# Kernel tuning notes

Hardware: AMD Instinct MI355X
Metric: run time of the kernel (lower is better)

Reference implementation:

```python
import jax, jax.numpy as jnp
import numpy as np

N_NODES = 35
N_EDGES = 1190
N_VIEWS = 6
C1_IN, C1_OUT = 1, 256
C2_IN, C2_OUT = 256, 256
C3_IN, C3_OUT = 256, 64


def _nnconv(x, edge_attr, src, dst, nn_w, nn_b, lin_w, bias, c_in, c_out):
    """PyG NNConv with aggr='mean': per-edge MLP weight, gather-matvec-scatter."""
    # per-edge weight matrices: [E, c_in, c_out]
    W = jax.nn.relu(edge_attr @ nn_w.T + nn_b).reshape(-1, c_in, c_out)
    # gather source features and apply per-edge weight: [E, c_out]
    msg = jnp.einsum('ei,eio->eo', x[src], W)
    # scatter-mean into target nodes
    agg = jax.ops.segment_sum(msg, dst, num_segments=N_NODES)
    cnt = jax.ops.segment_sum(jnp.ones((msg.shape[0],), msg.dtype), dst,
                              num_segments=N_NODES)
    agg = agg / jnp.maximum(cnt, 1.0)[:, None]
    # root transform (lin has no bias in PyG) + conv bias
    return agg + x @ lin_w.T + bias


def setup_inputs() -> dict:
    key = jax.random.key(0)
    ks = jax.random.split(key, 16)
    s = 0.05
    x = jnp.ones((N_NODES, C1_IN), jnp.float32)
    edge_attr = jax.random.uniform(ks[0], (N_EDGES, N_VIEWS), jnp.float32)
    edge_index = jax.random.randint(ks[1], (2, N_EDGES), 0, N_NODES, jnp.int32)
    inp = {
        'x': x, 'edge_attr': edge_attr, 'edge_index': edge_index,
        'nn1_w': jax.random.normal(ks[2], (C1_IN * C1_OUT, N_VIEWS), jnp.float32) * s,
        'nn1_b': jax.random.normal(ks[3], (C1_IN * C1_OUT,), jnp.float32) * s,
        'lin1_w': jax.random.normal(ks[4], (C1_OUT, C1_IN), jnp.float32) * s,
        'b1': jax.random.normal(ks[5], (C1_OUT,), jnp.float32) * s,
        'nn2_w': jax.random.normal(ks[6], (C2_IN * C2_OUT, N_VIEWS), jnp.float32) * s,
        'nn2_b': jax.random.normal(ks[7], (C2_IN * C2_OUT,), jnp.float32) * s,
        'lin2_w': jax.random.normal(ks[8], (C2_OUT, C2_IN), jnp.float32) * s,
        'b2': jax.random.normal(ks[9], (C2_OUT,), jnp.float32) * s,
        'nn3_w': jax.random.normal(ks[10], (C3_IN * C3_OUT, N_VIEWS), jnp.float32) * s,
        'nn3_b': jax.random.normal(ks[11], (C3_IN * C3_OUT,), jnp.float32) * s,
        'lin3_w': jax.random.normal(ks[12], (C3_OUT, C3_IN), jnp.float32) * s,
        'b3': jax.random.normal(ks[13], (C3_OUT,), jnp.float32) * s,
    }
    return inp


def reference(x, edge_attr, edge_index, nn1_w, nn1_b, lin1_w, b1,
              nn2_w, nn2_b, lin2_w, b2, nn3_w, nn3_b, lin3_w, b3):
    src, dst = edge_index[0], edge_index[1]
    x = jax.nn.relu(_nnconv(x, edge_attr, src, dst, nn1_w, nn1_b, lin1_w, b1, C1_IN, C1_OUT))
    x = jax.nn.relu(_nnconv(x, edge_attr, src, dst, nn2_w, nn2_b, lin2_w, b2, C2_IN, C2_OUT))
    x = jax.nn.relu(_nnconv(x, edge_attr, src, dst, nn3_w, nn3_b, lin3_w, b3, C3_IN, C3_OUT))
    # CBT: pairwise L1 distances over feature dim -> [N, N]
    # (equivalent to repeat(35,1,1) / transpose / abs / sum since N == 35)
    cbt = jnp.abs(x[None, :, :] - x[:, None, :]).sum(-1)
    return cbt
```

## Files before the change

### kernel.cpp

```cpp
#include <hip/hip_runtime.h>


#define NN 35
#define NE 1190
#define TE 10
#define NG 119

#define OFF_AGG1 0
#define OFF_AGG2 8960
#define OFF_AGG3 17920
#define OFF_CNT  20160
#define ZERO_N   20195
#define OFF_L2T  20224
#define OFF_X2M  85760
#define OFF_X3   94720

__global__ __launch_bounds__(256) void prep_k(float* __restrict__ ws,
                                              const float* __restrict__ lin2) {
    int b = blockIdx.x, t = threadIdx.x;
    if (b < 80) {
        int idx = b * 256 + t;
        if (idx < ZERO_N) ws[idx] = 0.f;
    } else {
        int i = b - 80;
        ws[OFF_L2T + i * 256 + t] = lin2[t * 256 + i];
    }
}

__global__ __launch_bounds__(512) void msg1_k(
    const float* __restrict__ x, const float* __restrict__ ea,
    const int* __restrict__ ei, const float* __restrict__ w1,
    const float* __restrict__ b1w, float* __restrict__ agg1,
    float* __restrict__ cnt) {
    int tid = threadIdx.x;
    int e = blockIdx.x * 2 + (tid >> 8);
    int o = tid & 255;
    int src = ei[e];
    int dst = ei[NE + e];
    float xs = x[src];
    const float* eap = ea + e * 6;
    const float* w = w1 + o * 6;
    float d = b1w[o];
#pragma unroll
    for (int v = 0; v < 6; v++) d = fmaf(eap[v], w[v], d);
    atomicAdd(agg1 + dst * 256 + o, xs * fmaxf(d, 0.f));
    if (o == 0) atomicAdd(cnt + dst, 1.0f);
}

__global__ __launch_bounds__(512, 4) void msg2x1_k(
    const float* __restrict__ x, const float* __restrict__ ea,
    const int* __restrict__ ei, const float* __restrict__ lin1,
    const float* __restrict__ b1, const float* __restrict__ agg1,
    const float* __restrict__ cnt, const float* __restrict__ w2,
    const float* __restrict__ b2w, float* __restrict__ agg2) {
    __shared__ float xs[TE][256];
    __shared__ float eas[TE][6];
    __shared__ int srcs[TE], dsts[TE];
    __shared__ float part[7][TE][64];
    int tid = threadIdx.x;
    int eg = blockIdx.x >> 2, og = blockIdx.x & 3;
    int e0 = eg * TE;
    if (tid < TE) { srcs[tid] = ei[e0 + tid]; dsts[tid] = ei[NE + e0 + tid]; }
    if (tid >= 64 && tid < 64 + TE * 6) {
        int t = tid - 64;
        eas[t / 6][t % 6] = ea[e0 * 6 + t];
    }
    __syncthreads();
    for (int idx = tid; idx < TE * 256; idx += 512) {
        int te = idx >> 8, i = idx & 255;
        int s = srcs[te];
        float c = fmaxf(cnt[s], 1.f);
        float v = agg1[s * 256 + i] / c + x[s] * lin1[i] + b1[i];
        xs[te][i] = fmaxf(v, 0.f);
    }
    __syncthreads();
    int ol = tid & 63;
    int o = og * 64 + ol;
    int ic = tid >> 6;
    float eareg[TE][6];
#pragma unroll
    for (int te = 0; te < TE; te++)
#pragma unroll
        for (int v = 0; v < 6; v++) eareg[te][v] = eas[te][v];
    float acc[TE] = {};
    for (int ii = 0; ii < 32; ii++) {
        int i = ic * 32 + ii;
        const float* w = w2 + (size_t)(i * 256 + o) * 6;
        float2 wa = *(const float2*)w;
        float2 wb = *(const float2*)(w + 2);
        float2 wc = *(const float2*)(w + 4);
        float b = b2w[i * 256 + o];
#pragma unroll
        for (int te = 0; te < TE; te += 2) {
            float dx = b, dy = b;
            dx = fmaf(eareg[te][0], wa.x, dx); dy = fmaf(eareg[te + 1][0], wa.x, dy);
            dx = fmaf(eareg[te][1], wa.y, dx); dy = fmaf(eareg[te + 1][1], wa.y, dy);
            dx = fmaf(eareg[te][2], wb.x, dx); dy = fmaf(eareg[te + 1][2], wb.x, dy);
            dx = fmaf(eareg[te][3], wb.y, dx); dy = fmaf(eareg[te + 1][3], wb.y, dy);
            dx = fmaf(eareg[te][4], wc.x, dx); dy = fmaf(eareg[te + 1][4], wc.x, dy);
            dx = fmaf(eareg[te][5], wc.y, dx); dy = fmaf(eareg[te + 1][5], wc.y, dy);
            dx = fmaxf(dx, 0.f);               dy = fmaxf(dy, 0.f);
            acc[te] = fmaf(xs[te][i], dx, acc[te]);
            acc[te + 1] = fmaf(xs[te + 1][i], dy, acc[te + 1]);
        }
    }
    if (ic > 0) {
#pragma unroll
        for (int te = 0; te < TE; te++) part[ic - 1][te][ol] = acc[te];
    }
    __syncthreads();
    if (ic == 0) {
#pragma unroll
        for (int te = 0; te < TE; te++) {
            float s = acc[te];
#pragma unroll
            for (int p = 0; p < 7; p++) s += part[p][te][ol];
            atomicAdd(agg2 + dsts[te] * 256 + o, s);
        }
    }
}

__global__ __launch_bounds__(512, 4) void msg3x2_k(
    const float* __restrict__ x, const float* __restrict__ ea,
    const int* __restrict__ ei, const float* __restrict__ lin1,
    const float* __restrict__ b1, const float* __restrict__ agg1,
    const float* __restrict__ cnt, const float* __restrict__ lin2T,
    const float* __restrict__ b2, const float* __restrict__ agg2,
    const float* __restrict__ w3, const float* __restrict__ b3w,
    float* __restrict__ agg3, float* __restrict__ x2m) {
    __shared__ float x1r[TE][256];
    __shared__ float xs[TE][64];
    __shared__ float eas[TE][6];
    __shared__ int srcs[TE], dsts[TE];
    __shared__ float part[7][TE][64];
    int tid = threadIdx.x;

    if (blockIdx.x >= 476) {
        int n = blockIdx.x - 476;
        float c = fmaxf(cnt[n], 1.f);
        if (tid < 256) {
            float v = agg1[n * 256 + tid] / c + x[n] * lin1[tid] + b1[tid];
            x1r[0][tid] = fmaxf(v, 0.f);
        }
        __syncthreads();
        int o = tid & 255, ic = tid >> 8;
        float s = 0.f;
        for (int ii = 0; ii < 128; ii++) {
            int i = ic * 128 + ii;
            s = fmaf(lin2T[i * 256 + o], x1r[0][i], s);
        }
        float* p2 = &part[0][0][0];
        if (ic == 1) p2[o] = s;
        __syncthreads();
        if (ic == 0) {
            float v = agg2[n * 256 + o] / c + s + p2[o] + b2[o];
            x2m[n * 256 + o] = fmaxf(v, 0.f);
        }
        return;
    }

    int eg = blockIdx.x >> 2, ig = blockIdx.x & 3;
    int e0 = eg * TE;
    if (tid < TE) { srcs[tid] = ei[e0 + tid]; dsts[tid] = ei[NE + e0 + tid]; }
    if (tid >= 64 && tid < 64 + TE * 6) {
        int t = tid - 64;
        eas[t / 6][t % 6] = ea[e0 * 6 + t];
    }
    __syncthreads();
    for (int idx = tid; idx < TE * 256; idx += 512) {
        int te = idx >> 8, i = idx & 255;
        int s = srcs[te];
        float c = fmaxf(cnt[s], 1.f);
        float v = agg1[s * 256 + i] / c + x[s] * lin1[i] + b1[i];
        x1r[te][i] = fmaxf(v, 0.f);
    }
    __syncthreads();
    int ol = tid & 63;
    int ic = tid >> 6;
    int o2 = ig * 64 + ol;
    {
        float acc2[TE] = {};
        for (int ii = 0; ii < 32; ii++) {
            int i = ic * 32 + ii;
            float w = lin2T[i * 256 + o2];
#pragma unroll
            for (int te = 0; te < TE; te++)
                acc2[te] = fmaf(w, x1r[te][i], acc2[te]);
        }
        if (ic > 0) {
#pragma unroll
            for (int te = 0; te < TE; te++) part[ic - 1][te][ol] = acc2[te];
        }
        __syncthreads();
        if (ic == 0) {
#pragma unroll
            for (int te = 0; te < TE; te++) {
                float ssum = acc2[te];
#pragma unroll
                for (int p = 0; p < 7; p++) ssum += part[p][te][ol];
                int s = srcs[te];
                float c = fmaxf(cnt[s], 1.f);
                float v = agg2[s * 256 + o2] / c + ssum + b2[o2];
                xs[te][ol] = fmaxf(v, 0.f);
            }
        }
        __syncthreads();
    }
    float eareg[TE][6];
#pragma unroll
    for (int te = 0; te < TE; te++)
#pragma unroll
        for (int v = 0; v < 6; v++) eareg[te][v] = eas[te][v];
    float acc[TE] = {};
    for (int jj = 0; jj < 8; jj++) {
        int ii = ic * 8 + jj;
        int i = ig * 64 + ii;
        const float* w = w3 + (size_t)(i * 64 + ol) * 6;
        float2 wa = *(const float2*)w;
        float2 wb = *(const float2*)(w + 2);
        float2 wc = *(const float2*)(w + 4);
        float b = b3w[i * 64 + ol];
#pragma unroll
        for (int te = 0; te < TE; te += 2) {
            float dx = b, dy = b;
            dx = fmaf(eareg[te][0], wa.x, dx); dy = fmaf(eareg[te + 1][0], wa.x, dy);
            dx = fmaf(eareg[te][1], wa.y, dx); dy = fmaf(eareg[te + 1][1], wa.y, dy);
            dx = fmaf(eareg[te][2], wb.x, dx); dy = fmaf(eareg[te + 1][2], wb.x, dy);
            dx = fmaf(eareg[te][3], wb.y, dx); dy = fmaf(eareg[te + 1][3], wb.y, dy);
            dx = fmaf(eareg[te][4], wc.x, dx); dy = fmaf(eareg[te + 1][4], wc.x, dy);
            dx = fmaf(eareg[te][5], wc.y, dx); dy = fmaf(eareg[te + 1][5], wc.y, dy);
            dx = fmaxf(dx, 0.f);               dy = fmaxf(dy, 0.f);
            acc[te] = fmaf(xs[te][ii], dx, acc[te]);
            acc[te + 1] = fmaf(xs[te + 1][ii], dy, acc[te + 1]);
        }
    }
    if (ic > 0) {
#pragma unroll
        for (int te = 0; te < TE; te++) part[ic - 1][te][ol] = acc[te];
    }
    __syncthreads();
    if (ic == 0) {
#pragma unroll
        for (int te = 0; te < TE; te++) {
            float s = acc[te];
#pragma unroll
            for (int p = 0; p < 7; p++) s += part[p][te][ol];
            atomicAdd(agg3 + dsts[te] * 64 + ol, s);
        }
    }
}

__global__ __launch_bounds__(256) void x3_k(
    const float* __restrict__ x2m, const float* __restrict__ lin3,
    const float* __restrict__ b3, const float* __restrict__ agg3,
    const float* __restrict__ cnt, float* __restrict__ x3) {
    __shared__ float xr[256];
    __shared__ float part[3][64];
    int n = blockIdx.x, tid = threadIdx.x;
    int o = tid & 63, ic = tid >> 6;
    xr[tid] = x2m[n * 256 + tid];
    __syncthreads();
    const float4* w = (const float4*)(lin3 + (size_t)o * 256 + ic * 64);
    float s = 0.f;
#pragma unroll
    for (int k = 0; k < 16; k++) {
        float4 wv = w[k];
        int i = ic * 64 + k * 4;
        s = fmaf(wv.x, xr[i], s);
        s = fmaf(wv.y, xr[i + 1], s);
        s = fmaf(wv.z, xr[i + 2], s);
        s = fmaf(wv.w, xr[i + 3], s);
    }
    if (ic > 0) part[ic - 1][o] = s;
    __syncthreads();
    if (ic == 0) {
        float tot = s + part[0][o] + part[1][o] + part[2][o];
        float c = fmaxf(cnt[n], 1.f);
        x3[n * 64 + o] = fmaxf(agg3[n * 64 + o] / c + tot + b3[o], 0.f);
    }
}

__global__ __launch_bounds__(256) void cbt_k(const float* __restrict__ x3,
                                             float* __restrict__ out) {
    int t = blockIdx.x * 256 + threadIdx.x;
    if (t >= NN * NN) return;
    int i = t / NN, j = t % NN;
    const float* a = x3 + i * 64;
    const float* b = x3 + j * 64;
    float s = 0.f;
#pragma unroll
    for (int f = 0; f < 64; f++) s += fabsf(a[f] - b[f]);
    out[t] = s;
}

extern "C" void kernel_launch(void* const* d_in, const int* in_sizes, int n_in,
                              void* d_out, int out_size, void* d_ws, size_t ws_size,
                              hipStream_t stream) {
    const float* x    = (const float*)d_in[0];
    const float* ea   = (const float*)d_in[1];
    const int*   ei   = (const int*)d_in[2];
    const float* nn1w = (const float*)d_in[3];
    const float* nn1b = (const float*)d_in[4];
    const float* lin1 = (const float*)d_in[5];
    const float* b1   = (const float*)d_in[6];
    const float* nn2w = (const float*)d_in[7];
    const float* nn2b = (const float*)d_in[8];
    const float* lin2 = (const float*)d_in[9];
    const float* b2   = (const float*)d_in[10];
    const float* nn3w = (const float*)d_in[11];
    const float* nn3b = (const float*)d_in[12];
    const float* lin3 = (const float*)d_in[13];
    const float* b3   = (const float*)d_in[14];

    float* ws    = (float*)d_ws;
    float* agg1  = ws + OFF_AGG1;
    float* agg2  = ws + OFF_AGG2;
    float* agg3  = ws + OFF_AGG3;
    float* cnt   = ws + OFF_CNT;
    float* lin2T = ws + OFF_L2T;
    float* x2m   = ws + OFF_X2M;
    float* x3v   = ws + OFF_X3;
    float* out   = (float*)d_out;

    prep_k<<<336, 256, 0, stream>>>(ws, lin2);
    msg1_k<<<NE / 2, 512, 0, stream>>>(x, ea, ei, nn1w, nn1b, agg1, cnt);
    msg2x1_k<<<NG * 4, 512, 0, stream>>>(x, ea, ei, lin1, b1, agg1, cnt,
                                         nn2w, nn2b, agg2);
    msg3x2_k<<<NG * 4 + NN, 512, 0, stream>>>(x, ea, ei, lin1, b1, agg1, cnt,
                                              lin2T, b2, agg2, nn3w, nn3b,
                                              agg3, x2m);
    x3_k<<<NN, 256, 0, stream>>>(x2m, lin3, b3, agg3, cnt, x3v);
    cbt_k<<<(NN * NN + 255) / 256, 256, 0, stream>>>(x3v, out);
}
```

Before: 140.9 us.

## Fuse all NNConv stages into one persistent kernel with grid barriers

Replaces the six-kernel pipeline with a single persistent kernel of 238 blocks that passes through the stages using software grid barriers on an atomic counter, plus a tiny init kernel to reset the counter. Float atomics for scatter-mean are replaced by per-destination edge lists built with ballot, with per-edge messages written to workspace and gathered deterministically by destination. The layer-2 root transform no longer needs a transposed copy of lin2. This targets launch overhead and atomic contention, at the cost of spin-wait barriers that rely on all blocks being co-resident, plus extra workspace traffic for the message buffers.

```diff
diff --git a/kernel.cpp b/kernel.cpp
--- a/kernel.cpp
+++ b/kernel.cpp
@@ -3,299 +3,307 @@
 
 #define NN 35
 #define NE 1190
-#define TE 10
-#define NG 119
-
-#define OFF_AGG1 0
-#define OFF_AGG2 8960
-#define OFF_AGG3 17920
-#define OFF_CNT  20160
-#define ZERO_N   20195
-#define OFF_L2T  20224
-#define OFF_X2M  85760
-#define OFF_X3   94720
-
-__global__ __launch_bounds__(256) void prep_k(float* __restrict__ ws,
-                                              const float* __restrict__ lin2) {
-    int b = blockIdx.x, t = threadIdx.x;
-    if (b < 80) {
-        int idx = b * 256 + t;
-        if (idx < ZERO_N) ws[idx] = 0.f;
-    } else {
-        int i = b - 80;
-        ws[OFF_L2T + i * 256 + t] = lin2[t * 256 + i];
-    }
+#define NBLK 238
+#define TE2 10
+#define TE3 5
+
+#define OFF_X1    64
+#define OFF_CNT   9024
+#define OFF_ELIST 9088
+#define OFF_MP    51200
+#define OFF_MP3   660480
+#define OFF_X2    736640
+#define OFF_X3    745600
+
+__global__ __launch_bounds__(64) void init_k(unsigned* bar) {
+    if (threadIdx.x < 16) bar[threadIdx.x] = 0u;
 }
 
-__global__ __launch_bounds__(512) void msg1_k(
-    const float* __restrict__ x, const float* __restrict__ ea,
-    const int* __restrict__ ei, const float* __restrict__ w1,
-    const float* __restrict__ b1w, float* __restrict__ agg1,
-    float* __restrict__ cnt) {
-    int tid = threadIdx.x;
-    int e = blockIdx.x * 2 + (tid >> 8);
-    int o = tid & 255;
-    int src = ei[e];
-    int dst = ei[NE + e];
-    float xs = x[src];
-    const float* eap = ea + e * 6;
-    const float* w = w1 + o * 6;
-    float d = b1w[o];
-#pragma unroll
-    for (int v = 0; v < 6; v++) d = fmaf(eap[v], w[v], d);
-    atomicAdd(agg1 + dst * 256 + o, xs * fmaxf(d, 0.f));
-    if (o == 0) atomicAdd(cnt + dst, 1.0f);
+__device__ __forceinline__ void gbar(unsigned* bar, unsigned target) {
+    __syncthreads();
+    if (threadIdx.x == 0) {
+        __threadfence();
+        atomicAdd(bar, 1u);
+        while (__hip_atomic_load(bar, __ATOMIC_RELAXED,
+                                 __HIP_MEMORY_SCOPE_AGENT) < target)
+            __builtin_amdgcn_s_sleep(2);
+        __threadfence();
+    }
+    __syncthreads();
 }
 
-__global__ __launch_bounds__(512, 4) void msg2x1_k(
-    const float* __restrict__ x, const float* __restrict__ ea,
-    const int* __restrict__ ei, const float* __restrict__ lin1,
-    const float* __restrict__ b1, const float* __restrict__ agg1,
-    const float* __restrict__ cnt, const float* __restrict__ w2,
-    const float* __restrict__ b2w, float* __restrict__ agg2) {
-    __shared__ float xs[TE][256];
-    __shared__ float eas[TE][6];
-    __shared__ int srcs[TE], dsts[TE];
-    __shared__ float part[7][TE][64];
-    int tid = threadIdx.x;
-    int eg = blockIdx.x >> 2, og = blockIdx.x & 3;
-    int e0 = eg * TE;
-    if (tid < TE) { srcs[tid] = ei[e0 + tid]; dsts[tid] = ei[NE + e0 + tid]; }
-    if (tid >= 64 && tid < 64 + TE * 6) {
-        int t = tid - 64;
-        eas[t / 6][t % 6] = ea[e0 * 6 + t];
-    }
-    __syncthreads();
-    for (int idx = tid; idx < TE * 256; idx += 512) {
-        int te = idx >> 8, i = idx & 255;
-        int s = srcs[te];
-        float c = fmaxf(cnt[s], 1.f);
-        float v = agg1[s * 256 + i] / c + x[s] * lin1[i] + b1[i];
-        xs[te][i] = fmaxf(v, 0.f);
-    }
-    __syncthreads();
-    int ol = tid & 63;
-    int o = og * 64 + ol;
-    int ic = tid >> 6;
-    float eareg[TE][6];
-#pragma unroll
-    for (int te = 0; te < TE; te++)
-#pragma unroll
-        for (int v = 0; v < 6; v++) eareg[te][v] = eas[te][v];
-    float acc[TE] = {};
-    for (int ii = 0; ii < 32; ii++) {
-        int i = ic * 32 + ii;
-        const float* w = w2 + (size_t)(i * 256 + o) * 6;
-        float2 wa = *(const float2*)w;
-        float2 wb = *(const float2*)(w + 2);
-        float2 wc = *(const float2*)(w + 4);
-        float b = b2w[i * 256 + o];
-#pragma unroll
-        for (int te = 0; te < TE; te += 2) {
-            float dx = b, dy = b;
-            dx = fmaf(eareg[te][0], wa.x, dx); dy = fmaf(eareg[te + 1][0], wa.x, dy);
-            dx = fmaf(eareg[te][1], wa.y, dx); dy = fmaf(eareg[te + 1][1], wa.y, dy);
-            dx = fmaf(eareg[te][2], wb.x, dx); dy = fmaf(eareg[te + 1][2], wb.x, dy);
-            dx = fmaf(eareg[te][3], wb.y, dx); dy = fmaf(eareg[te + 1][3], wb.y, dy);
-            dx = fmaf(eareg[te][4], wc.x, dx); dy = fmaf(eareg[te + 1][4], wc.x, dy);
-            dx = fmaf(eareg[te][5], wc.y, dx); dy = fmaf(eareg[te + 1][5], wc.y, dy);
-            dx = fmaxf(dx, 0.f);               dy = fmaxf(dy, 0.f);
-            acc[te] = fmaf(xs[te][i], dx, acc[te]);
-            acc[te + 1] = fmaf(xs[te + 1][i], dy, acc[te + 1]);
-        }
-    }
-    if (ic > 0) {
-#pragma unroll
-        for (int te = 0; te < TE; te++) part[ic - 1][te][ol] = acc[te];
-    }
-    __syncthreads();
-    if (ic == 0) {
-#pragma unroll
-        for (int te = 0; te < TE; te++) {
-            float s = acc[te];
-#pragma unroll
-            for (int p = 0; p < 7; p++) s += part[p][te][ol];
-            atomicAdd(agg2 + dsts[te] * 256 + o, s);
-        }
-    }
-}
-
-__global__ __launch_bounds__(512, 4) void msg3x2_k(
-    const float* __restrict__ x, const float* __restrict__ ea,
-    const int* __restrict__ ei, const float* __restrict__ lin1,
-    const float* __restrict__ b1, const float* __restrict__ agg1,
-    const float* __restrict__ cnt, const float* __restrict__ lin2T,
-    const float* __restrict__ b2, const float* __restrict__ agg2,
+__global__ __launch_bounds__(512, 2) void mega_k(
+    float* __restrict__ ws, const float* __restrict__ x,
+    const float* __restrict__ ea, const int* __restrict__ ei,
+    const float* __restrict__ w1, const float* __restrict__ b1w,
+    const float* __restrict__ lin1, const float* __restrict__ b1,
+    const float* __restrict__ w2, const float* __restrict__ b2w,
+    const float* __restrict__ lin2, const float* __restrict__ b2,
     const float* __restrict__ w3, const float* __restrict__ b3w,
-    float* __restrict__ agg3, float* __restrict__ x2m) {
-    __shared__ float x1r[TE][256];
-    __shared__ float xs[TE][64];
-    __shared__ float eas[TE][6];
-    __shared__ int srcs[TE], dsts[TE];
-    __shared__ float part[7][TE][64];
-    int tid = threadIdx.x;
-
-    if (blockIdx.x >= 476) {
-        int n = blockIdx.x - 476;
-        float c = fmaxf(cnt[n], 1.f);
-        if (tid < 256) {
-            float v = agg1[n * 256 + tid] / c + x[n] * lin1[tid] + b1[tid];
-            x1r[0][tid] = fmaxf(v, 0.f);
-        }
-        __syncthreads();
-        int o = tid & 255, ic = tid >> 8;
-        float s = 0.f;
-        for (int ii = 0; ii < 128; ii++) {
-            int i = ic * 128 + ii;
-            s = fmaf(lin2T[i * 256 + o], x1r[0][i], s);
-        }
-        float* p2 = &part[0][0][0];
-        if (ic == 1) p2[o] = s;
+    const float* __restrict__ lin3, const float* __restrict__ b3,
+    float* __restrict__ out) {
+    __shared__ float smem[4096];
+    unsigned* bar = (unsigned*)ws;
+    const int tid = threadIdx.x;
+    const int bid = blockIdx.x;
+    int* elist_all = (int*)(ws + OFF_ELIST);
+
+    if (bid < NN) {
+        const int n = bid;
+        int* elist = elist_all + n * NE;
+        int* degS = (int*)smem;
+        if (tid < 64) {
+            int deg = 0;
+            for (int base = 0; base < NE; base += 64) {
+                const int e = base + tid;
+                const bool m = (e < NE) && (ei[NE + e] == n);
+                const unsigned long long mk = __ballot(m);
+                if (m) elist[deg + __popcll(mk & ((1ull << tid) - 1ull))] = e;
+                deg += __popcll(mk);
+            }
+            if (tid == 0) { degS[0] = deg; ws[OFF_CNT + n] = (float)deg; }
+        }
+        __syncthreads();
+        const int deg = degS[0];
+        const int o = tid & 255, ech = tid >> 8;
+        const float* wr = w1 + o * 6;
+        const float wv0 = wr[0], wv1 = wr[1], wv2 = wr[2];
+        const float wv3 = wr[3], wv4 = wr[4], wv5 = wr[5];
+        const float bb = b1w[o];
+        float a = 0.f;
+        for (int k = ech; k < deg; k += 2) {
+            const int e = elist[k];
+            const float* eap = ea + e * 6;
+            float d = bb;
+            d = fmaf(eap[0], wv0, d); d = fmaf(eap[1], wv1, d);
+            d = fmaf(eap[2], wv2, d); d = fmaf(eap[3], wv3, d);
+            d = fmaf(eap[4], wv4, d); d = fmaf(eap[5], wv5, d);
+            a = fmaf(x[ei[e]], fmaxf(d, 0.f), a);
+        }
+        float* part = smem + 1024;
+        if (ech == 1) part[o] = a;
+        __syncthreads();
+        if (ech == 0) {
+            const float c = fmaxf((float)deg, 1.f);
+            const float v = (a + part[o]) / c + x[n] * lin1[o] + b1[o];
+            ws[OFF_X1 + n * 256 + o] = fmaxf(v, 0.f);
+        }
+    }
+    gbar(bar, NBLK * 1u);
+
+    {
+        const int eg = bid >> 1, ig = bid & 1;
+        const int e0 = eg * TE2;
+        int* srcsS = (int*)smem;
+        float* easS = smem + 16;
+        float* xsS = smem + 128;
+        float* partS = smem + 1536;
+        if (tid < TE2) srcsS[tid] = ei[e0 + tid];
+        if (tid >= 64 && tid < 64 + TE2 * 6) {
+            const int t = tid - 64;
+            easS[t] = ea[e0 * 6 + t];
+        }
+        __syncthreads();
+        for (int idx = tid; idx < TE2 * 128; idx += 512) {
+            const int te = idx >> 7, il = idx & 127;
+            xsS[te * 128 + il] = ws[OFF_X1 + srcsS[te] * 256 + ig * 128 + il];
+        }
+        __syncthreads();
+        const int o = tid & 255, ich = tid >> 8;
+        float ear[TE2][6];
+#pragma unroll
+        for (int te = 0; te < TE2; te++)
+#pragma unroll
+            for (int v = 0; v < 6; v++) ear[te][v] = easS[te * 6 + v];
+        float acc[TE2] = {};
+        for (int ii = 0; ii < 64; ii++) {
+            const int il = ich * 64 + ii;
+            const int i = ig * 128 + il;
+            const float* wp = w2 + (size_t)(i * 256 + o) * 6;
+            const float2 wa = *(const float2*)wp;
+            const float2 wb = *(const float2*)(wp + 2);
+            const float2 wc = *(const float2*)(wp + 4);
+            const float b = b2w[i * 256 + o];
+#pragma unroll
+            for (int te = 0; te < TE2; te += 2) {
+                float dx = b, dy = b;
+                dx = fmaf(ear[te][0], wa.x, dx); dy = fmaf(ear[te+1][0], wa.x, dy);
+                dx = fmaf(ear[te][1], wa.y, dx); dy = fmaf(ear[te+1][1], wa.y, dy);
+                dx = fmaf(ear[te][2], wb.x, dx); dy = fmaf(ear[te+1][2], wb.x, dy);
+                dx = fmaf(ear[te][3], wb.y, dx); dy = fmaf(ear[te+1][3], wb.y, dy);
+                dx = fmaf(ear[te][4], wc.x, dx); dy = fmaf(ear[te+1][4], wc.x, dy);
+                dx = fmaf(ear[te][5], wc.y, dx); dy = fmaf(ear[te+1][5], wc.y, dy);
+                dx = fmaxf(dx, 0.f);             dy = fmaxf(dy, 0.f);
+                acc[te]   = fmaf(xsS[te * 128 + il], dx, acc[te]);
+                acc[te+1] = fmaf(xsS[(te+1) * 128 + il], dy, acc[te+1]);
+            }
+        }
+        if (ich == 1) {
+#pragma unroll
+            for (int te = 0; te < TE2; te++) partS[te * 256 + o] = acc[te];
+        }
+        __syncthreads();
+        if (ich == 0) {
+#pragma unroll
+            for (int te = 0; te < TE2; te++)
+                ws[OFF_MP + (size_t)(ig * NE + e0 + te) * 256 + o] =
+                    acc[te] + partS[te * 256 + o];
+        }
+    }
+    gbar(bar, NBLK * 2u);
+
+    if (bid < NN) {
+        const int n = bid;
+        const int deg = (int)ws[OFF_CNT + n];
+        const int* el = elist_all + n * NE;
+        float* xrowS = smem;
+        float* pA = smem + 256;
+        float* pB = smem + 512;
+        if (tid < 256) xrowS[tid] = ws[OFF_X1 + n * 256 + tid];
+        __syncthreads();
+        const int o = tid & 255, ich = tid >> 8;
+        const float4* l4 = (const float4*)(lin2 + (size_t)o * 256 + ich * 128);
+        float slin = 0.f;
+#pragma unroll
+        for (int k = 0; k < 32; k++) {
+            const float4 wv = l4[k];
+            const int i = ich * 128 + k * 4;
+            slin = fmaf(wv.x, xrowS[i], slin);
+            slin = fmaf(wv.y, xrowS[i+1], slin);
+            slin = fmaf(wv.z, xrowS[i+2], slin);
+            slin = fmaf(wv.w, xrowS[i+3], slin);
+        }
+        float sagg = 0.f;
+        const float* mpb = ws + OFF_MP + (size_t)ich * NE * 256;
+        for (int k = 0; k < deg; k++)
+            sagg += mpb[(size_t)el[k] * 256 + o];
+        if (ich == 1) { pA[o] = slin; pB[o] = sagg; }
+        __syncthreads();
+        if (ich == 0) {
+            const float c = fmaxf((float)deg, 1.f);
+            const float v = (sagg + pB[o]) / c + slin + pA[o] + b2[o];
+            ws[OFF_X2 + n * 256 + o] = fmaxf(v, 0.f);
+        }
+    }
+    gbar(bar, NBLK * 3u);
+
+    {
+        const int e0 = bid * TE3;
+        int* srcsS = (int*)smem;
+        float* easS = smem + 8;
+        float* xsS = smem + 256;
+        float* partS = smem + 1536;
+        if (tid < TE3) srcsS[tid] = ei[e0 + tid];
+        if (tid >= 64 && tid < 64 + TE3 * 6) {
+            const int t = tid - 64;
+            easS[t] = ea[e0 * 6 + t];
+        }
+        __syncthreads();
+        for (int idx = tid; idx < TE3 * 256; idx += 512) {
+            const int te = idx >> 8, il = idx & 255;
+            xsS[te * 256 + il] = ws[OFF_X2 + srcsS[te] * 256 + il];
+        }
+        __syncthreads();
+        const int o3 = tid & 63, ic = tid >> 6;
+        float ear[TE3][6];
+#pragma unroll
+        for (int te = 0; te < TE3; te++)
+#pragma unroll
+            for (int v = 0; v < 6; v++) ear[te][v] = easS[te * 6 + v];
+        float acc[TE3] = {};
+        for (int ii = 0; ii < 32; ii++) {
+            const int i = ic * 32 + ii;
+            const float* wp = w3 + (size_t)(i * 64 + o3) * 6;
+            const float2 wa = *(const float2*)wp;
+            const float2 wb = *(const float2*)(wp + 2);
+            const float2 wc = *(const float2*)(wp + 4);
+            const float b = b3w[i * 64 + o3];
+#pragma unroll
+            for (int te = 0; te < TE3; te++) {
+                float d = b;
+                d = fmaf(ear[te][0], wa.x, d);
+                d = fmaf(ear[te][1], wa.y, d);
+                d = fmaf(ear[te][2], wb.x, d);
+                d = fmaf(ear[te][3], wb.y, d);
+                d = fmaf(ear[te][4], wc.x, d);
+                d = fmaf(ear[te][5], wc.y, d);
+                acc[te] = fmaf(xsS[te * 256 + i], fmaxf(d, 0.f), acc[te]);
+            }
+        }
+        if (ic > 0) {
+#pragma unroll
+            for (int te = 0; te < TE3; te++)
+                partS[(ic - 1) * 320 + te * 64 + o3] = acc[te];
+        }
         __syncthreads();
         if (ic == 0) {
-            float v = agg2[n * 256 + o] / c + s + p2[o] + b2[o];
-            x2m[n * 256 + o] = fmaxf(v, 0.f);
-        }
-        return;
-    }
-
-    int eg = blockIdx.x >> 2, ig = blockIdx.x & 3;
-    int e0 = eg * TE;
-    if (tid < TE) { srcs[tid] = ei[e0 + tid]; dsts[tid] = ei[NE + e0 + tid]; }
-    if (tid >= 64 && tid < 64 + TE * 6) {
-        int t = tid - 64;
-        eas[t / 6][t % 6] = ea[e0 * 6 + t];
-    }
-    __syncthreads();
-    for (int idx = tid; idx < TE * 256; idx += 512) {
-        int te = idx >> 8, i = idx & 255;
-        int s = srcs[te];
-        float c = fmaxf(cnt[s], 1.f);
-        float v = agg1[s * 256 + i] / c + x[s] * lin1[i] + b1[i];
-        x1r[te][i] = fmaxf(v, 0.f);
-    }
-    __syncthreads();
-    int ol = tid & 63;
-    int ic = tid >> 6;
-    int o2 = ig * 64 + ol;
-    {
-        float acc2[TE] = {};
-        for (int ii = 0; ii < 32; ii++) {
-            int i = ic * 32 + ii;
-            float w = lin2T[i * 256 + o2];
-#pragma unroll
-            for (int te = 0; te < TE; te++)
-                acc2[te] = fmaf(w, x1r[te][i], acc2[te]);
-        }
-        if (ic > 0) {
-#pragma unroll
-            for (int te = 0; te < TE; te++) part[ic - 1][te][ol] = acc2[te];
-        }
+#pragma unroll
+            for (int te = 0; te < TE3; te++) {
+                float s = acc[te];
+#pragma unroll
+                for (int p = 0; p < 7; p++) s += partS[p * 320 + te * 64 + o3];
+                ws[OFF_MP3 + (size_t)(e0 + te) * 64 + o3] = s;
+            }
+        }
+    }
+    gbar(bar, NBLK * 4u);
+
+    if (bid < NN) {
+        const int n = bid;
+        const int deg = (int)ws[OFF_CNT + n];
+        const int* el = elist_all + n * NE;
+        float* x2S = smem;
+        float* pL = smem + 256;
+        float* pG = smem + 768;
+        if (tid < 256) x2S[tid] = ws[OFF_X2 + n * 256 + tid];
+        __syncthreads();
+        const int o3 = tid & 63, ic = tid >> 6;
+        const float4* l4 = (const float4*)(lin3 + (size_t)o3 * 256 + ic * 32);
+        float slin = 0.f;
+#pragma unroll
+        for (int k = 0; k < 8; k++) {
+            const float4 wv = l4[k];
+            const int i = ic * 32 + k * 4;
+            slin = fmaf(wv.x, x2S[i], slin);
+            slin = fmaf(wv.y, x2S[i+1], slin);
+            slin = fmaf(wv.z, x2S[i+2], slin);
+            slin = fmaf(wv.w, x2S[i+3], slin);
+        }
+        float sagg = 0.f;
+        for (int k = ic; k < deg; k += 8)
+            sagg += ws[OFF_MP3 + (size_t)el[k] * 64 + o3];
+        if (ic > 0) { pL[(ic-1) * 64 + o3] = slin; pG[(ic-1) * 64 + o3] = sagg; }
         __syncthreads();
         if (ic == 0) {
-#pragma unroll
-            for (int te = 0; te < TE; te++) {
-                float ssum = acc2[te];
-#pragma unroll
-                for (int p = 0; p < 7; p++) ssum += part[p][te][ol];
-                int s = srcs[te];
-                float c = fmaxf(cnt[s], 1.f);
-                float v = agg2[s * 256 + o2] / c + ssum + b2[o2];
-                xs[te][ol] = fmaxf(v, 0.f);
-            }
-        }
-        __syncthreads();
-    }
-    float eareg[TE][6];
-#pragma unroll
-    for (int te = 0; te < TE; te++)
-#pragma unroll
-        for (int v = 0; v < 6; v++) eareg[te][v] = eas[te][v];
-    float acc[TE] = {};
-    for (int jj = 0; jj < 8; jj++) {
-        int ii = ic * 8 + jj;
-        int i = ig * 64 + ii;
-        const float* w = w3 + (size_t)(i * 64 + ol) * 6;
-        float2 wa = *(const float2*)w;
-        float2 wb = *(const float2*)(w + 2);
-        float2 wc = *(const float2*)(w + 4);
-        float b = b3w[i * 64 + ol];
-#pragma unroll
-        for (int te = 0; te < TE; te += 2) {
-            float dx = b, dy = b;
-            dx = fmaf(eareg[te][0], wa.x, dx); dy = fmaf(eareg[te + 1][0], wa.x, dy);
-            dx = fmaf(eareg[te][1], wa.y, dx); dy = fmaf(eareg[te + 1][1], wa.y, dy);
-            dx = fmaf(eareg[te][2], wb.x, dx); dy = fmaf(eareg[te + 1][2], wb.x, dy);
-            dx = fmaf(eareg[te][3], wb.y, dx); dy = fmaf(eareg[te + 1][3], wb.y, dy);
-            dx = fmaf(eareg[te][4], wc.x, dx); dy = fmaf(eareg[te + 1][4], wc.x, dy);
-            dx = fmaf(eareg[te][5], wc.y, dx); dy = fmaf(eareg[te + 1][5], wc.y, dy);
-            dx = fmaxf(dx, 0.f);               dy = fmaxf(dy, 0.f);
-            acc[te] = fmaf(xs[te][ii], dx, acc[te]);
-            acc[te + 1] = fmaf(xs[te + 1][ii], dy, acc[te + 1]);
-        }
-    }
-    if (ic > 0) {
-#pragma unroll
-        for (int te = 0; te < TE; te++) part[ic - 1][te][ol] = acc[te];
-    }
-    __syncthreads();
-    if (ic == 0) {
-#pragma unroll
-        for (int te = 0; te < TE; te++) {
-            float s = acc[te];
-#pragma unroll
-            for (int p = 0; p < 7; p++) s += part[p][te][ol];
-            atomicAdd(agg3 + dsts[te] * 64 + ol, s);
-        }
-    }
-}
-
-__global__ __launch_bounds__(256) void x3_k(
-    const float* __restrict__ x2m, const float* __restrict__ lin3,
-    const float* __restrict__ b3, const float* __restrict__ agg3,
-    const float* __restrict__ cnt, float* __restrict__ x3) {
-    __shared__ float xr[256];
-    __shared__ float part[3][64];
-    int n = blockIdx.x, tid = threadIdx.x;
-    int o = tid & 63, ic = tid >> 6;
-    xr[tid] = x2m[n * 256 + tid];
-    __syncthreads();
-    const float4* w = (const float4*)(lin3 + (size_t)o * 256 + ic * 64);
-    float s = 0.f;
-#pragma unroll
-    for (int k = 0; k < 16; k++) {
-        float4 wv = w[k];
-        int i = ic * 64 + k * 4;
-        s = fmaf(wv.x, xr[i], s);
-        s = fmaf(wv.y, xr[i + 1], s);
-        s = fmaf(wv.z, xr[i + 2], s);
-        s = fmaf(wv.w, xr[i + 3], s);
-    }
-    if (ic > 0) part[ic - 1][o] = s;
-    __syncthreads();
-    if (ic == 0) {
-        float tot = s + part[0][o] + part[1][o] + part[2][o];
-        float c = fmaxf(cnt[n], 1.f);
-        x3[n * 64 + o] = fmaxf(agg3[n * 64 + o] / c + tot + b3[o], 0.f);
-    }
-}
-
-__global__ __launch_bounds__(256) void cbt_k(const float* __restrict__ x3,
-                                             float* __restrict__ out) {
-    int t = blockIdx.x * 256 + threadIdx.x;
-    if (t >= NN * NN) return;
-    int i = t / NN, j = t % NN;
-    const float* a = x3 + i * 64;
-    const float* b = x3 + j * 64;
-    float s = 0.f;
-#pragma unroll
-    for (int f = 0; f < 64; f++) s += fabsf(a[f] - b[f]);
-    out[t] = s;
+            float sl = slin, sg = sagg;
+#pragma unroll
+            for (int p = 0; p < 7; p++) { sl += pL[p*64+o3]; sg += pG[p*64+o3]; }
+            const float c = fmaxf((float)deg, 1.f);
+            ws[OFF_X3 + n * 64 + o3] = fmaxf(sg / c + sl + b3[o3], 0.f);
+        }
+    }
+    gbar(bar, NBLK * 5u);
+
+    if (bid < NN) {
+        const int i = bid;
+        float* sx = smem;
+        for (int idx = tid; idx < NN * 64; idx += 512) sx[idx] = ws[OFF_X3 + idx];
+        __syncthreads();
+        const int f = tid & 63, jg = tid >> 6;
+        const float xi = sx[i * 64 + f];
+        for (int j = jg; j < NN; j += 8) {
+            float d = fabsf(xi - sx[j * 64 + f]);
+#pragma unroll
+            for (int off = 32; off > 0; off >>= 1) d += __shfl_xor(d, off);
+            if (f == 0) out[i * NN + j] = d;
+        }
+    }
 }
 
 extern "C" void kernel_launch(void* const* d_in, const int* in_sizes, int n_in,
                               void* d_out, int out_size, void* d_ws, size_t ws_size,
                               hipStream_t stream) {
+    (void)in_sizes; (void)n_in; (void)out_size; (void)ws_size;
     const float* x    = (const float*)d_in[0];
     const float* ea   = (const float*)d_in[1];
     const int*   ei   = (const int*)d_in[2];
@@ -312,23 +320,9 @@
     const float* lin3 = (const float*)d_in[13];
     const float* b3   = (const float*)d_in[14];
 
-    float* ws    = (float*)d_ws;
-    float* agg1  = ws + OFF_AGG1;
-    float* agg2  = ws + OFF_AGG2;
-    float* agg3  = ws + OFF_AGG3;
-    float* cnt   = ws + OFF_CNT;
-    float* lin2T = ws + OFF_L2T;
-    float* x2m   = ws + OFF_X2M;
-    float* x3v   = ws + OFF_X3;
-    float* out   = (float*)d_out;
-
-    prep_k<<<336, 256, 0, stream>>>(ws, lin2);
-    msg1_k<<<NE / 2, 512, 0, stream>>>(x, ea, ei, nn1w, nn1b, agg1, cnt);
-    msg2x1_k<<<NG * 4, 512, 0, stream>>>(x, ea, ei, lin1, b1, agg1, cnt,
-                                         nn2w, nn2b, agg2);
-    msg3x2_k<<<NG * 4 + NN, 512, 0, stream>>>(x, ea, ei, lin1, b1, agg1, cnt,
-                                              lin2T, b2, agg2, nn3w, nn3b,
-                                              agg3, x2m);
-    x3_k<<<NN, 256, 0, stream>>>(x2m, lin3, b3, agg3, cnt, x3v);
-    cbt_k<<<(NN * NN + 255) / 256, 256, 0, stream>>>(x3v, out);
+    float* ws = (float*)d_ws;
+    init_k<<<1, 64, 0, stream>>>((unsigned*)d_ws);
+    mega_k<<<NBLK, 512, 0, stream>>>(ws, x, ea, ei, nn1w, nn1b, lin1, b1,
+                                     nn2w, nn2b, lin2, b2, nn3w, nn3b,
+                                     lin3, b3, (float*)d_out);
 }
```

Result: slower. 252.5 us (+79.2%).
